# Kernel tuning notes

Measured on AMD Instinct MI355X. Metric: run time of the kernel, lower is better.

## Reference

```python
import jax, jax.numpy as jnp
import numpy as np

HIDDEN = 128
N_ING = 20000
N_CMP = 10000
N_EDGE = 1000000


def setup_inputs() -> dict:
    key = jax.random.key(0)
    k1, k2, k3, k4, k5, k6, k7 = jax.random.split(key, 7)
    x_ingredient = jax.random.normal(k1, (N_ING, HIDDEN), dtype=jnp.float32)
    x_compound = jax.random.normal(k2, (N_CMP, HIDDEN), dtype=jnp.float32)
    src_idx = jax.random.randint(k3, (N_EDGE,), 0, N_ING)
    dst_idx = jax.random.randint(k4, (N_EDGE,), 0, N_CMP)
    edge_index = jnp.stack([src_idx, dst_idx], axis=0)  # [2, E]
    # Linear(2H, H) then Linear(H, 1), PyTorch default init scale ~ 1/sqrt(fan_in)
    s1 = 1.0 / np.sqrt(2 * HIDDEN)
    s2 = 1.0 / np.sqrt(HIDDEN)
    W1 = jax.random.uniform(k5, (2 * HIDDEN, HIDDEN), dtype=jnp.float32, minval=-s1, maxval=s1)
    b1 = jax.random.uniform(k6, (HIDDEN,), dtype=jnp.float32, minval=-s1, maxval=s1)
    W2 = jax.random.uniform(k7, (HIDDEN, 1), dtype=jnp.float32, minval=-s2, maxval=s2)
    b2 = jnp.zeros((1,), dtype=jnp.float32)
    return {"x_ingredient": x_ingredient, "x_compound": x_compound,
            "edge_index": edge_index, "W1": W1, "b1": b1, "W2": W2, "b2": b2}


def reference(x_ingredient, x_compound, edge_index, W1, b1, W2, b2):
    src = x_ingredient[edge_index[0]]  # [E, H] gather
    dst = x_compound[edge_index[1]]    # [E, H] gather
    h = jnp.concatenate([src, dst], axis=-1)          # [E, 2H]
    h = jax.nn.relu(jnp.dot(h, W1) + b1)              # [E, H]
    out = jax.nn.sigmoid(jnp.dot(h, W2) + b2)         # [E, 1]
    return out
```

## Files before the change

### kernel.cpp

```cpp
#include <hip/hip_runtime.h>


#define H  128
#define NI 20000
#define NC 10000
#define NE 1000000

typedef _Float16 half8   __attribute__((ext_vector_type(8)));
typedef float    floatx2 __attribute__((ext_vector_type(2)));
typedef float    floatx4 __attribute__((ext_vector_type(4)));

#define P8_OFF    0
#define Q8_OFF    (NI * H)

#define PB (NI / 16)
#define QB (NC / 16)
#define NSTRIP 4
#define PBLKS ((PB + NSTRIP - 1) / NSTRIP)
#define QBLKS ((QB + NSTRIP - 1) / NSTRIP)

#if __has_builtin(__builtin_amdgcn_cvt_pk_f32_fp8) && __has_builtin(__builtin_amdgcn_cvt_pk_fp8_f32)
#define HW_FP8 1
#else
#define HW_FP8 0
__device__ inline unsigned char enc_e4m3(float x) {
    unsigned s = x < 0.0f ? 0x80u : 0u;
    float a = fminf(fabsf(x), 448.0f);
    if (a < 0.0009765625f) return (unsigned char)s;
    int e; float m = frexpf(a, &e);
    int E = e + 6;
    if (E <= 0) {
        int f = (int)rintf(a * 512.0f);
        if (f > 7) return (unsigned char)(s | 0x08);
        return (unsigned char)(s | f);
    }
    int f = (int)rintf((m * 2.0f - 1.0f) * 8.0f);
    if (f == 8) { f = 0; ++E; }
    if (E > 15 || (E == 15 && f > 6)) { E = 15; f = 6; }
    return (unsigned char)(s | (E << 3) | f);
}
__device__ inline float dec_e4m3(unsigned char b) {
    int E = (b >> 3) & 15, f = b & 7;
    float v = (E == 0) ? (float)f * 0.001953125f
                       : (float)(8 + f) * exp2f((float)(E - 10));
    return (b & 0x80) ? -v : v;
}
#endif

__device__ inline floatx2 relu2(floatx2 v) {
#if __has_builtin(__builtin_elementwise_max)
    floatx2 z = {0.0f, 0.0f};
    return __builtin_elementwise_max(v, z);
#else
    floatx2 r = { fmaxf(v.x, 0.0f), fmaxf(v.y, 0.0f) };
    return r;
#endif
}

__device__ __forceinline__ float fast_sigmoid(float x) {
#if __has_builtin(__builtin_amdgcn_exp2f) && __has_builtin(__builtin_amdgcn_rcpf)
    const float t = __builtin_amdgcn_exp2f(-1.4426950408889634f * x);
    return __builtin_amdgcn_rcpf(1.0f + t);
#else
    return 1.0f / (1.0f + __expf(-x));
#endif
}

__launch_bounds__(256)
__global__ void pq_gemm(const float* __restrict__ xin,
                        const float* __restrict__ xcmp,
                        const float* __restrict__ b1,
                        const float* __restrict__ W1,
                        unsigned char* __restrict__ wsb) {
    const int b    = blockIdx.x;
    const bool isQ = (b >= PBLKS);
    const int  sb  = isQ ? b - PBLKS : b;
    const int  s0  = sb * NSTRIP;
    const int  smax = (isQ ? QB : PB) - 1;
    const float* X = isQ ? xcmp : xin;
    unsigned char* OUT8 = wsb + (isQ ? Q8_OFF : P8_OFF);

    const int lane = threadIdx.x & 63;
    const int w    = threadIdx.x >> 6;
    const int quad = lane >> 4;
    const int m    = lane & 15;

    half8 bf[2][4];
    float b1v[2];
#pragma unroll
    for (int nt = 0; nt < 2; ++nt) {
        const int n = w * 32 + nt * 16 + m;
#pragma unroll
        for (int ks = 0; ks < 4; ++ks) {
            const float* wp = W1 + (long)(isQ * 128 + ks * 32 + quad * 8) * H + n;
            half8 v;
#pragma unroll
            for (int j = 0; j < 8; ++j)
                v[j] = (_Float16)wp[j * H];
            bf[nt][ks] = v;
        }
        b1v[nt] = isQ ? b1[n] : 0.0f;
    }

#define LOADA(S, AF) do {                                                \
        const int _s = (S) > smax ? smax : (S);                          \
        const float* xr = X + (long)(_s * 16 + m) * H + quad * 8;        \
        _Pragma("unroll")                                                \
        for (int ks = 0; ks < 4; ++ks) {                                 \
            float4 a = *(const float4*)(xr + ks * 32);                   \
            float4 c = *(const float4*)(xr + ks * 32 + 4);               \
            half8 v = { (_Float16)a.x, (_Float16)a.y, (_Float16)a.z,     \
                        (_Float16)a.w, (_Float16)c.x, (_Float16)c.y,     \
                        (_Float16)c.z, (_Float16)c.w };                  \
            AF[ks] = v;                                                  \
        }                                                                \
    } while (0)

#if HW_FP8
#define EMIT8(PTR, V) do {                                               \
        const unsigned _u = (unsigned)__builtin_amdgcn_cvt_pk_fp8_f32((V), (V), 0, false); \
        *(unsigned char*)(PTR) = (unsigned char)(_u & 0xff);             \
    } while (0)
#else
#define EMIT8(PTR, V) do { *(unsigned char*)(PTR) = enc_e4m3(V); } while (0)
#endif

#define STRIPC(S, AF) do {                                               \
        floatx4 acc[2] = { (floatx4)0.0f, (floatx4)0.0f };               \
        _Pragma("unroll")                                                \
        for (int ks = 0; ks < 4; ++ks)                                   \
            _Pragma("unroll")                                            \
            for (int nt = 0; nt < 2; ++nt)                               \
                acc[nt] = __builtin_amdgcn_mfma_f32_16x16x32_f16(        \
                              AF[ks], bf[nt][ks], acc[nt], 0, 0, 0);     \
        if ((S) <= smax) {                                               \
            const int rb = (S) * 16;                                     \
            _Pragma("unroll")                                            \
            for (int nt = 0; nt < 2; ++nt) {                             \
                const int col = w * 32 + nt * 16 + m;                    \
                _Pragma("unroll")                                        \
                for (int r = 0; r < 4; ++r) {                            \
                    const float v = acc[nt][r] + b1v[nt];                \
                    EMIT8(OUT8 + (rb + quad * 4 + r) * H + col, v);      \
                }                                                        \
            }                                                            \
        }                                                                \
    } while (0)

    half8 afA[4], afB[4];
    LOADA(s0, afA);
    LOADA(s0 + 1, afB);
    STRIPC(s0,     afA);
    LOADA(s0 + 2, afA);
    STRIPC(s0 + 1, afB);
    LOADA(s0 + 3, afB);
    STRIPC(s0 + 2, afA);
    STRIPC(s0 + 3, afB);

#undef LOADA
#undef STRIPC
#undef EMIT8
}

#define EGRID 2048
#define ESTEP (32 * EGRID)

__launch_bounds__(256)
__global__ void edge_mlp(const unsigned char* __restrict__ wsb,
                         const int* __restrict__ src_idx,
                         const int* __restrict__ dst_idx,
                         const float* __restrict__ W2,
                         const float* __restrict__ b2p,
                         float* __restrict__ out) {
    const int tid  = threadIdx.x;
    const int c    = tid & 7;
    const int slot = tid >> 3;

    floatx2 w2v[8];
#pragma unroll
    for (int i = 0; i < 8; ++i) w2v[i] = *(const floatx2*)(W2 + c * 16 + i * 2);
    const float b2v = b2p[0];

    const unsigned char* P8 = wsb + P8_OFF;
    const unsigned char* Q8 = wsb + Q8_OFF;
    const int ebase = blockIdx.x * 32 + slot;

#define LDIDX(K, SI, DI) do {                                        \
        int _e = ebase + (K) * ESTEP;                                \
        _e = _e < NE ? _e : NE - 1;                                  \
        SI = __builtin_nontemporal_load(src_idx + _e);               \
        DI = __builtin_nontemporal_load(dst_idx + _e);               \
    } while (0)

#define GATHER(SI, DI, PD, QD) do {                                  \
        PD = *(const uint4*)(P8 + (SI) * H + c * 16);                \
        QD = *(const uint4*)(Q8 + (DI) * H + c * 16);                \
    } while (0)

#if HW_FP8
#define DECODE(PW, QW, PL, PH, QL, QH) do {                          \
        PL = __builtin_amdgcn_cvt_pk_f32_fp8((int)(PW), false);      \
        PH = __builtin_amdgcn_cvt_pk_f32_fp8((int)(PW), true);       \
        QL = __builtin_amdgcn_cvt_pk_f32_fp8((int)(QW), false);      \
        QH = __builtin_amdgcn_cvt_pk_f32_fp8((int)(QW), true);       \
    } while (0)
#else
#define DECODE(PW, QW, PL, PH, QL, QH) do {                          \
        PL = { dec_e4m3((PW) & 0xff), dec_e4m3(((PW) >> 8) & 0xff) };  \
        PH = { dec_e4m3(((PW) >> 16) & 0xff), dec_e4m3((PW) >> 24) };  \
        QL = { dec_e4m3((QW) & 0xff), dec_e4m3(((QW) >> 8) & 0xff) };  \
        QH = { dec_e4m3(((QW) >> 16) & 0xff), dec_e4m3((QW) >> 24) };  \
    } while (0)
#endif

#define COMPUTE(K, PD, QD, MASKED) do {                              \
        floatx2 acc2 = {0.0f, 0.0f};                                 \
        const unsigned pw[4] = { PD.x, PD.y, PD.z, PD.w };           \
        const unsigned qw[4] = { QD.x, QD.y, QD.z, QD.w };           \
        _Pragma("unroll")                                            \
        for (int jw = 0; jw < 4; ++jw) {                             \
            floatx2 pl, ph, ql, qh;                                  \
            DECODE(pw[jw], qw[jw], pl, ph, ql, qh);                  \
            acc2 += relu2(pl + ql) * w2v[2 * jw];                    \
            acc2 += relu2(ph + qh) * w2v[2 * jw + 1];                \
        }                                                            \
        float acc = acc2.x + acc2.y;                                 \
        acc += __shfl_xor(acc, 1);                                   \
        acc += __shfl_xor(acc, 2);                                   \
        acc += __shfl_xor(acc, 4);                                   \
        const int _e = ebase + (K) * ESTEP;                          \
        if (c == 0 && (!(MASKED) || _e < NE)) {                      \
            const float r = fast_sigmoid(acc + b2v);                 \
            __builtin_nontemporal_store(r, out + _e);                \
        }                                                            \
    } while (0)

    int siA, diA, siB, diB, si2, di2, si3, di3;
    uint4 pdA, qdA, pdB, qdB;
    LDIDX(0, siA, diA);
    LDIDX(1, siB, diB);
    GATHER(siA, diA, pdA, qdA);
    GATHER(siB, diB, pdB, qdB);
    LDIDX(2, si2, di2);
    LDIDX(3, si3, di3);

#pragma unroll 1
    for (int i = 0; i < 7; ++i) {
        const int k = 2 * i;
        uint4 pdC, qdC, pdD, qdD;
        GATHER(si2, di2, pdC, qdC);
        GATHER(si3, di3, pdD, qdD);
        LDIDX(k + 4, si2, di2);
        LDIDX(k + 5, si3, di3);
        COMPUTE(k,     pdA, qdA, false);
        COMPUTE(k + 1, pdB, qdB, false);
        pdA = pdC; qdA = qdC; pdB = pdD; qdB = qdD;
    }

    COMPUTE(14, pdA, qdA, false);
    COMPUTE(15, pdB, qdB, true);

#undef LDIDX
#undef GATHER
#undef COMPUTE
#undef DECODE
}

extern "C" void kernel_launch(void* const* d_in, const int* in_sizes, int n_in,
                              void* d_out, int out_size, void* d_ws, size_t ws_size,
                              hipStream_t stream) {
    const float* xin  = (const float*)d_in[0];
    const float* xcmp = (const float*)d_in[1];
    const int*   eidx = (const int*)d_in[2];
    const float* W1   = (const float*)d_in[3];
    const float* b1   = (const float*)d_in[4];
    const float* W2   = (const float*)d_in[5];
    const float* b2   = (const float*)d_in[6];
    float* out = (float*)d_out;
    unsigned char* wsb = (unsigned char*)d_ws;

    hipLaunchKernelGGL(pq_gemm, dim3(PBLKS + QBLKS), dim3(256), 0, stream,
                       xin, xcmp, b1, W1, wsb);
    hipLaunchKernelGGL(edge_mlp, dim3(EGRID), dim3(256), 0, stream,
                       wsb, eidx, eidx + NE, W2, b2, out);
}
```

Before: 109.7 us.

## Fully unroll edge loop with deeper gather prefetch and DPP reductions

```diff
diff --git a/kernel.cpp b/kernel.cpp
--- a/kernel.cpp
+++ b/kernel.cpp
@@ -65,6 +65,25 @@
     return 1.0f / (1.0f + __expf(-x));
 #endif
 }
+
+#if __has_builtin(__builtin_amdgcn_update_dpp)
+template <int CTRL>
+__device__ __forceinline__ float dpp_add(float x) {
+    const int yi = __builtin_amdgcn_update_dpp(0, __float_as_int(x), CTRL, 0xf, 0xf, false);
+    return x + __int_as_float(yi);
+}
+#define REDUCE8(ACC) do {                          \
+        ACC = dpp_add<0xB1>(ACC);          \
+        ACC = dpp_add<0x4E>(ACC);          \
+        ACC = dpp_add<0x141>(ACC);         \
+    } while (0)
+#else
+#define REDUCE8(ACC) do {                          \
+        ACC += __shfl_xor(ACC, 1);                 \
+        ACC += __shfl_xor(ACC, 2);                 \
+        ACC += __shfl_xor(ACC, 4);                 \
+    } while (0)
+#endif
 
 __launch_bounds__(256)
 __global__ void pq_gemm(const float* __restrict__ xin,
@@ -185,16 +204,19 @@
     const unsigned char* Q8 = wsb + Q8_OFF;
     const int ebase = blockIdx.x * 32 + slot;
 
-#define LDIDX(K, SI, DI) do {                                        \
+    int  si[16], di[16];
+    uint4 pd[16], qd[16];
+
+#define LDIDX(K) do {                                                \
         int _e = ebase + (K) * ESTEP;                                \
-        _e = _e < NE ? _e : NE - 1;                                  \
-        SI = __builtin_nontemporal_load(src_idx + _e);               \
-        DI = __builtin_nontemporal_load(dst_idx + _e);               \
-    } while (0)
-
-#define GATHER(SI, DI, PD, QD) do {                                  \
-        PD = *(const uint4*)(P8 + (SI) * H + c * 16);                \
-        QD = *(const uint4*)(Q8 + (DI) * H + c * 16);                \
+        if ((K) == 15) _e = _e < NE ? _e : NE - 1;                   \
+        si[K] = __builtin_nontemporal_load(src_idx + _e);            \
+        di[K] = __builtin_nontemporal_load(dst_idx + _e);            \
+    } while (0)
+
+#define ISSUE(K) do {                                                \
+        pd[K] = *(const uint4*)(P8 + si[K] * H + c * 16);            \
+        qd[K] = *(const uint4*)(Q8 + di[K] * H + c * 16);            \
     } while (0)
 
 #if HW_FP8
@@ -213,10 +235,10 @@
     } while (0)
 #endif
 
-#define COMPUTE(K, PD, QD, MASKED) do {                              \
+#define COMPUTE(K) do {                                              \
         floatx2 acc2 = {0.0f, 0.0f};                                 \
-        const unsigned pw[4] = { PD.x, PD.y, PD.z, PD.w };           \
-        const unsigned qw[4] = { QD.x, QD.y, QD.z, QD.w };           \
+        const unsigned pw[4] = { pd[K].x, pd[K].y, pd[K].z, pd[K].w }; \
+        const unsigned qw[4] = { qd[K].x, qd[K].y, qd[K].z, qd[K].w }; \
         _Pragma("unroll")                                            \
         for (int jw = 0; jw < 4; ++jw) {                             \
             floatx2 pl, ph, ql, qh;                                  \
@@ -225,43 +247,26 @@
             acc2 += relu2(ph + qh) * w2v[2 * jw + 1];                \
         }                                                            \
         float acc = acc2.x + acc2.y;                                 \
-        acc += __shfl_xor(acc, 1);                                   \
-        acc += __shfl_xor(acc, 2);                                   \
-        acc += __shfl_xor(acc, 4);                                   \
+        REDUCE8(acc);                                                \
+        const float r = fast_sigmoid(acc + b2v);   \
         const int _e = ebase + (K) * ESTEP;                          \
-        if (c == 0 && (!(MASKED) || _e < NE)) {                      \
-            const float r = fast_sigmoid(acc + b2v);                 \
+        if (c == 0 && ((K) < 15 || _e < NE))                         \
             __builtin_nontemporal_store(r, out + _e);                \
-        }                                                            \
-    } while (0)
-
-    int siA, diA, siB, diB, si2, di2, si3, di3;
-    uint4 pdA, qdA, pdB, qdB;
-    LDIDX(0, siA, diA);
-    LDIDX(1, siB, diB);
-    GATHER(siA, diA, pdA, qdA);
-    GATHER(siB, diB, pdB, qdB);
-    LDIDX(2, si2, di2);
-    LDIDX(3, si3, di3);
-
-#pragma unroll 1
-    for (int i = 0; i < 7; ++i) {
-        const int k = 2 * i;
-        uint4 pdC, qdC, pdD, qdD;
-        GATHER(si2, di2, pdC, qdC);
-        GATHER(si3, di3, pdD, qdD);
-        LDIDX(k + 4, si2, di2);
-        LDIDX(k + 5, si3, di3);
-        COMPUTE(k,     pdA, qdA, false);
-        COMPUTE(k + 1, pdB, qdB, false);
-        pdA = pdC; qdA = qdC; pdB = pdD; qdB = qdD;
+    } while (0)
+
+#pragma unroll
+    for (int k = 0; k < 8; ++k) LDIDX(k);
+#pragma unroll
+    for (int k = 0; k < 4; ++k) ISSUE(k);
+#pragma unroll
+    for (int k = 0; k < 16; ++k) {
+        if (k + 4 < 16) ISSUE(k + 4);
+        if (k + 8 < 16) LDIDX(k + 8);
+        COMPUTE(k);
     }
 
-    COMPUTE(14, pdA, qdA, false);
-    COMPUTE(15, pdB, qdB, true);
-
 #undef LDIDX
-#undef GATHER
+#undef ISSUE
 #undef COMPUTE
 #undef DECODE
 }
```

Result: no change. 107.8 us (-1.8%).
